# Performance work log

Hardware: AMD Instinct MI355X
Metric: run time of the kernel (lower is better)

## Reference

```python
import jax, jax.numpy as jnp
import numpy as np

L, B, H = 4096, 32, 512


def setup_inputs() -> dict:
    key = jax.random.key(0)
    k1, k2, k3, k4 = jax.random.split(key, 4)
    query = jax.random.normal(k1, (B, H), dtype=jnp.float32)
    key_val = jax.random.normal(k2, (L, B, H), dtype=jnp.float32)
    # torch Linear(2H, H, bias=False): weight is (H, 2H); we store transposed (2H, H)
    W = jax.random.normal(k3, (2 * H, H), dtype=jnp.float32) * (1.0 / np.sqrt(2 * H))
    v = jax.random.normal(k4, (H,), dtype=jnp.float32)
    return {"query": query, "key_val": key_val, "W": W, "v": v}


def reference(query, key_val, W, v):
    # concat([expand(query), key], -1) @ W == query @ W_q + key @ W_k
    Wq, Wk = W[:H], W[H:]                       # each (H, H)
    q_proj = query @ Wq                          # (B, H)
    k_proj = jnp.einsum('lbi,ih->lbh', key_val, Wk)  # (L, B, H)
    energy = jnp.tanh(q_proj[None, :, :] + k_proj)   # (L, B, H)
    scores = jnp.einsum('h,lbh->bl', v, energy)      # (B, L)
    return jax.nn.softmax(scores, axis=1)[:, None, :]  # (B, 1, L)
```

## Files before the change

kernel.cpp:

```cpp
#include <hip/hip_runtime.h>
#include <hip/hip_bf16.h>
#include <stdint.h>

#define L_DIM 4096
#define B_DIM 32
#define H_DIM 512
#define M_DIM (L_DIM * B_DIM)
#define K_DIM H_DIM

typedef _Float16 half8 __attribute__((ext_vector_type(8)));
typedef __fp16 fp16x2 __attribute__((ext_vector_type(2)));
typedef float floatx4 __attribute__((ext_vector_type(4)));

__device__ __forceinline__ float tanh_fast(float x) {
  float e = __builtin_amdgcn_exp2f(x * 2.88539008177793f);
  return 1.0f - 2.0f * __builtin_amdgcn_rcpf(e + 1.0f);
}

__device__ __forceinline__ uint2 pack4(const float4& f) {
  const fp16x2 p0 = __builtin_amdgcn_cvt_pkrtz(f.x, f.y);
  const fp16x2 p1 = __builtin_amdgcn_cvt_pkrtz(f.z, f.w);
  uint2 u;
  u.x = __builtin_bit_cast(unsigned, p0);
  u.y = __builtin_bit_cast(unsigned, p1);
  return u;
}

__global__ __launch_bounds__(128) void qproj_kernel(const float* __restrict__ query,
                                                    const float* __restrict__ W,
                                                    float* __restrict__ qp) {
  const int b = blockIdx.x;
  const int h = threadIdx.x * 4;
  const float* qrow = query + b * H_DIM;
  float4 acc = make_float4(0.f, 0.f, 0.f, 0.f);
#pragma unroll 8
  for (int i = 0; i < K_DIM; ++i) {
    const float qv = qrow[i];
    const float4 w4 = *(const float4*)(W + (size_t)i * H_DIM + h);
    acc.x += qv * w4.x; acc.y += qv * w4.y;
    acc.z += qv * w4.z; acc.w += qv * w4.w;
  }
  *(float4*)(qp + (size_t)b * H_DIM + h) = acc;
}

__global__ __launch_bounds__(256) void wconv_kernel(const float* __restrict__ W,
                                                    _Float16* __restrict__ W2) {
  const int t = blockIdx.x * 256 + threadIdx.x;
  const int l15 = t & 15;
  const int q = (t >> 4) & 3;
  const int nc = (t >> 6) & 31;
  const int kt = t >> 11;
  const int n = nc * 16 + l15;
  const int kbase = H_DIM + kt * 32 + q * 8;
  half8 h;
#pragma unroll
  for (int j = 0; j < 8; ++j)
    h[j] = (_Float16)W[(size_t)(kbase + j) * H_DIM + n];
  *(half8*)(W2 + (size_t)t * 8) = h;
}

__global__ __launch_bounds__(256, 2) void fused_gemm_kernel(
    const float* __restrict__ key, const _Float16* __restrict__ W2,
    const float* __restrict__ qp, const float* __restrict__ v,
    float* __restrict__ scores) {
  __shared__ __align__(16) _Float16 As[2][64 * 40];
  __shared__ float swave[256];

  const int tid = threadIdx.x;
  const int lane = tid & 63;
  const int w = tid >> 6;
  const int l15 = lane & 15;
  const int quad = lane >> 4;
  const int m0 = blockIdx.x * 64;

  const int ar = tid >> 3;
  const int aseg = tid & 7;
  const float* ag0 = key + (size_t)(m0 + ar) * K_DIM + aseg * 4;
  const float* ag1 = ag0 + (size_t)32 * K_DIM;
  const int adst0 = ar * 40 + aseg * 4;
  const int adst1 = (ar + 32) * 40 + aseg * 4;

  const half8* bptr = (const half8*)W2 + (size_t)(w * 8) * 64 + lane;

  int aoff[4];
#pragma unroll
  for (int fm = 0; fm < 4; ++fm) aoff[fm] = (fm * 16 + l15) * 40 + quad * 8;

  floatx4 acc[4][8];
#pragma unroll
  for (int fm = 0; fm < 4; ++fm)
#pragma unroll
    for (int fn = 0; fn < 8; ++fn) acc[fm][fn] = (floatx4)0.0f;

  float4 ra0 = *(const float4*)(ag0);
  float4 ra1 = *(const float4*)(ag1);
  half8 bn[8];
#pragma unroll
  for (int fn = 0; fn < 8; ++fn) bn[fn] = bptr[fn * 64];
  bptr += 32 * 64;
  *(uint2*)(As[0] + adst0) = pack4(ra0);
  *(uint2*)(As[0] + adst1) = pack4(ra1);
  ra0 = *(const float4*)(ag0 + 32);
  ra1 = *(const float4*)(ag1 + 32);
  __syncthreads();

  for (int kt = 0; kt < 16; ++kt) {
    half8 bc[8];
#pragma unroll
    for (int fn = 0; fn < 8; ++fn) bc[fn] = bn[fn];
    if (kt < 15) {
#pragma unroll
      for (int fn = 0; fn < 8; ++fn) bn[fn] = bptr[fn * 64];
      bptr += 32 * 64;
    }
    half8 av[4];
#pragma unroll
    for (int fm = 0; fm < 4; ++fm) av[fm] = *(const half8*)(As[kt & 1] + aoff[fm]);
    if (kt < 15) {
      _Float16* dst = As[(kt + 1) & 1];
      *(uint2*)(dst + adst0) = pack4(ra0);
      *(uint2*)(dst + adst1) = pack4(ra1);
      if (kt < 14) {
        ra0 = *(const float4*)(ag0 + (kt + 2) * 32);
        ra1 = *(const float4*)(ag1 + (kt + 2) * 32);
      }
    }
#pragma unroll
    for (int fm = 0; fm < 4; ++fm)
#pragma unroll
      for (int fn = 0; fn < 8; ++fn)
        acc[fm][fn] = __builtin_amdgcn_mfma_f32_16x16x32_f16(av[fm], bc[fn],
                                                             acc[fm][fn], 0, 0, 0);
    __syncthreads();
  }

  float vv[8];
#pragma unroll
  for (int fn = 0; fn < 8; ++fn) vv[fn] = v[w * 128 + fn * 16 + l15];

#pragma unroll
  for (int fm = 0; fm < 4; ++fm) {
#pragma unroll
    for (int r = 0; r < 4; ++r) {
      const int mrow = fm * 16 + quad * 4 + r;
      const float* qrow = qp + (size_t)(mrow & 31) * H_DIM;
      float rs = 0.f;
#pragma unroll
      for (int fn = 0; fn < 8; ++fn) {
        const int n = w * 128 + fn * 16 + l15;
        const float x = qrow[n] + acc[fm][fn][r];
        rs += vv[fn] * tanh_fast(x);
      }
      rs += __shfl_xor(rs, 1);
      rs += __shfl_xor(rs, 2);
      rs += __shfl_xor(rs, 4);
      rs += __shfl_xor(rs, 8);
      if (l15 == 0) swave[w * 64 + mrow] = rs;
    }
  }
  __syncthreads();
  if (tid < 64) {
    const float s = swave[tid] + swave[64 + tid] + swave[128 + tid] + swave[192 + tid];
    const int m = m0 + tid;
    scores[(size_t)(m & 31) * L_DIM + (m >> 5)] = s;
  }
}

__global__ __launch_bounds__(256) void softmax_kernel(const float* __restrict__ scores,
                                                      float* __restrict__ out) {
  const int b = blockIdx.x;
  const int t = threadIdx.x;
  __shared__ float red[256];
  const float* srow = scores + (size_t)b * L_DIM;
  float s[16];
#pragma unroll
  for (int i = 0; i < 16; ++i) s[i] = srow[t + i * 256];
  float mx = s[0];
#pragma unroll
  for (int i = 1; i < 16; ++i) mx = fmaxf(mx, s[i]);
  red[t] = mx;
  __syncthreads();
  for (int off = 128; off > 0; off >>= 1) {
    if (t < off) red[t] = fmaxf(red[t], red[t + off]);
    __syncthreads();
  }
  mx = red[0];
  __syncthreads();
  float sum = 0.f;
#pragma unroll
  for (int i = 0; i < 16; ++i) {
    s[i] = __builtin_amdgcn_exp2f((s[i] - mx) * 1.44269504f);
    sum += s[i];
  }
  red[t] = sum;
  __syncthreads();
  for (int off = 128; off > 0; off >>= 1) {
    if (t < off) red[t] += red[t + off];
    __syncthreads();
  }
  const float inv = 1.0f / red[0];
#pragma unroll
  for (int i = 0; i < 16; ++i) out[(size_t)b * L_DIM + t + i * 256] = s[i] * inv;
}

extern "C" void kernel_launch(void* const* d_in, const int* in_sizes, int n_in,
                              void* d_out, int out_size, void* d_ws, size_t ws_size,
                              hipStream_t stream) {
  const float* query = (const float*)d_in[0];
  const float* key   = (const float*)d_in[1];
  const float* W     = (const float*)d_in[2];
  const float* v     = (const float*)d_in[3];
  float* out = (float*)d_out;

  char* ws = (char*)d_ws;
  float* qp       = (float*)ws;
  float* scores   = (float*)(ws + 65536);
  _Float16* W2    = (_Float16*)(ws + 65536 + 524288);

  qproj_kernel<<<32, 128, 0, stream>>>(query, W, qp);
  wconv_kernel<<<128, 256, 0, stream>>>(W, W2);
  fused_gemm_kernel<<<M_DIM / 64, 256, 0, stream>>>(key, W2, qp, v, scores);
  softmax_kernel<<<B_DIM, 256, 0, stream>>>(scores, out);
}
```

Before: 446.7 us.

## Enlarge GEMM tile to 128 rows with 8 waves, merge prep kernels, shuffle softmax

The fused GEMM block grows from 64 to 128 rows and from 4 to 8 waves. Each wave now covers 64 output columns instead of 128, so the fp16 weight tile is loaded from L2 once per 128 rows rather than per 64. The query projection and weight conversion kernels are merged into one launch, and the softmax reductions switch from shared-memory trees to wavefront shuffles. In exchange, each block holds more LDS and more A-fragment registers, which may reduce occupancy.

```diff
diff --git a/kernel.cpp b/kernel.cpp
--- a/kernel.cpp
+++ b/kernel.cpp
@@ -26,77 +26,77 @@
   return u;
 }
 
-__global__ __launch_bounds__(128) void qproj_kernel(const float* __restrict__ query,
-                                                    const float* __restrict__ W,
-                                                    float* __restrict__ qp) {
-  const int b = blockIdx.x;
-  const int h = threadIdx.x * 4;
-  const float* qrow = query + b * H_DIM;
-  float4 acc = make_float4(0.f, 0.f, 0.f, 0.f);
+__global__ __launch_bounds__(256) void prep_kernel(const float* __restrict__ query,
+                                                   const float* __restrict__ W,
+                                                   float* __restrict__ qp,
+                                                   _Float16* __restrict__ W2) {
+  if (blockIdx.x < 128) {
+    const int t = blockIdx.x * 256 + threadIdx.x;
+    const int l15 = t & 15;
+    const int q = (t >> 4) & 3;
+    const int nc = (t >> 6) & 31;
+    const int kt = t >> 11;
+    const int n = nc * 16 + l15;
+    const int kbase = H_DIM + kt * 32 + q * 8;
+    half8 h;
+#pragma unroll
+    for (int j = 0; j < 8; ++j)
+      h[j] = (_Float16)W[(size_t)(kbase + j) * H_DIM + n];
+    *(half8*)(W2 + (size_t)t * 8) = h;
+  } else if (threadIdx.x < 128) {
+    const int b = blockIdx.x - 128;
+    const int h = threadIdx.x * 4;
+    const float* qrow = query + b * H_DIM;
+    float4 acc = make_float4(0.f, 0.f, 0.f, 0.f);
 #pragma unroll 8
-  for (int i = 0; i < K_DIM; ++i) {
-    const float qv = qrow[i];
-    const float4 w4 = *(const float4*)(W + (size_t)i * H_DIM + h);
-    acc.x += qv * w4.x; acc.y += qv * w4.y;
-    acc.z += qv * w4.z; acc.w += qv * w4.w;
-  }
-  *(float4*)(qp + (size_t)b * H_DIM + h) = acc;
-}
-
-__global__ __launch_bounds__(256) void wconv_kernel(const float* __restrict__ W,
-                                                    _Float16* __restrict__ W2) {
-  const int t = blockIdx.x * 256 + threadIdx.x;
-  const int l15 = t & 15;
-  const int q = (t >> 4) & 3;
-  const int nc = (t >> 6) & 31;
-  const int kt = t >> 11;
-  const int n = nc * 16 + l15;
-  const int kbase = H_DIM + kt * 32 + q * 8;
-  half8 h;
-#pragma unroll
-  for (int j = 0; j < 8; ++j)
-    h[j] = (_Float16)W[(size_t)(kbase + j) * H_DIM + n];
-  *(half8*)(W2 + (size_t)t * 8) = h;
-}
-
-__global__ __launch_bounds__(256, 2) void fused_gemm_kernel(
+    for (int i = 0; i < K_DIM; ++i) {
+      const float qv = qrow[i];
+      const float4 w4 = *(const float4*)(W + (size_t)i * H_DIM + h);
+      acc.x += qv * w4.x; acc.y += qv * w4.y;
+      acc.z += qv * w4.z; acc.w += qv * w4.w;
+    }
+    *(float4*)(qp + (size_t)b * H_DIM + h) = acc;
+  }
+}
+
+__global__ __launch_bounds__(512, 2) void fused_gemm_kernel(
     const float* __restrict__ key, const _Float16* __restrict__ W2,
     const float* __restrict__ qp, const float* __restrict__ v,
     float* __restrict__ scores) {
-  __shared__ __align__(16) _Float16 As[2][64 * 40];
-  __shared__ float swave[256];
+  __shared__ __align__(16) _Float16 As[2][128 * 40];
+  __shared__ float swave[8 * 128];
 
   const int tid = threadIdx.x;
   const int lane = tid & 63;
-  const int w = tid >> 6;
+  const int wn = tid >> 6;
   const int l15 = lane & 15;
   const int quad = lane >> 4;
-  const int m0 = blockIdx.x * 64;
+  const int m0 = blockIdx.x * 128;
 
   const int ar = tid >> 3;
   const int aseg = tid & 7;
   const float* ag0 = key + (size_t)(m0 + ar) * K_DIM + aseg * 4;
-  const float* ag1 = ag0 + (size_t)32 * K_DIM;
+  const float* ag1 = ag0 + (size_t)64 * K_DIM;
   const int adst0 = ar * 40 + aseg * 4;
-  const int adst1 = (ar + 32) * 40 + aseg * 4;
-
-  const half8* bptr = (const half8*)W2 + (size_t)(w * 8) * 64 + lane;
-
-  int aoff[4];
-#pragma unroll
-  for (int fm = 0; fm < 4; ++fm) aoff[fm] = (fm * 16 + l15) * 40 + quad * 8;
-
-  floatx4 acc[4][8];
-#pragma unroll
-  for (int fm = 0; fm < 4; ++fm)
-#pragma unroll
-    for (int fn = 0; fn < 8; ++fn) acc[fm][fn] = (floatx4)0.0f;
+  const int adst1 = (ar + 64) * 40 + aseg * 4;
+
+  const half8* bptr = (const half8*)W2 + (size_t)(wn * 4) * 64 + lane;
+
+  int aoff[8];
+#pragma unroll
+  for (int fm = 0; fm < 8; ++fm) aoff[fm] = (fm * 16 + l15) * 40 + quad * 8;
+
+  floatx4 acc[8][4];
+#pragma unroll
+  for (int fm = 0; fm < 8; ++fm)
+#pragma unroll
+    for (int fn = 0; fn < 4; ++fn) acc[fm][fn] = (floatx4)0.0f;
 
   float4 ra0 = *(const float4*)(ag0);
   float4 ra1 = *(const float4*)(ag1);
-  half8 bn[8];
-#pragma unroll
-  for (int fn = 0; fn < 8; ++fn) bn[fn] = bptr[fn * 64];
+  half8 bn[4];
+#pragma unroll
+  for (int fn = 0; fn < 4; ++fn) bn[fn] = bptr[fn * 64];
   bptr += 32 * 64;
   *(uint2*)(As[0] + adst0) = pack4(ra0);
   *(uint2*)(As[0] + adst1) = pack4(ra1);
@@ -105,17 +105,17 @@
   __syncthreads();
 
   for (int kt = 0; kt < 16; ++kt) {
-    half8 bc[8];
-#pragma unroll
-    for (int fn = 0; fn < 8; ++fn) bc[fn] = bn[fn];
+    half8 bc[4];
+#pragma unroll
+    for (int fn = 0; fn < 4; ++fn) bc[fn] = bn[fn];
     if (kt < 15) {
 #pragma unroll
-      for (int fn = 0; fn < 8; ++fn) bn[fn] = bptr[fn * 64];
+      for (int fn = 0; fn < 4; ++fn) bn[fn] = bptr[fn * 64];
       bptr += 32 * 64;
     }
-    half8 av[4];
-#pragma unroll
-    for (int fm = 0; fm < 4; ++fm) av[fm] = *(const half8*)(As[kt & 1] + aoff[fm]);
+    half8 av[8];
+#pragma unroll
+    for (int fm = 0; fm < 8; ++fm) av[fm] = *(const half8*)(As[kt & 1] + aoff[fm]);
     if (kt < 15) {
       _Float16* dst = As[(kt + 1) & 1];
       *(uint2*)(dst + adst0) = pack4(ra0);
@@ -126,28 +126,28 @@
       }
     }
 #pragma unroll
-    for (int fm = 0; fm < 4; ++fm)
-#pragma unroll
-      for (int fn = 0; fn < 8; ++fn)
+    for (int fm = 0; fm < 8; ++fm)
+#pragma unroll
+      for (int fn = 0; fn < 4; ++fn)
         acc[fm][fn] = __builtin_amdgcn_mfma_f32_16x16x32_f16(av[fm], bc[fn],
                                                              acc[fm][fn], 0, 0, 0);
     __syncthreads();
   }
 
-  float vv[8];
-#pragma unroll
-  for (int fn = 0; fn < 8; ++fn) vv[fn] = v[w * 128 + fn * 16 + l15];
-
-#pragma unroll
-  for (int fm = 0; fm < 4; ++fm) {
+  float vv[4];
+#pragma unroll
+  for (int fn = 0; fn < 4; ++fn) vv[fn] = v[wn * 64 + fn * 16 + l15];
+
+#pragma unroll
+  for (int fm = 0; fm < 8; ++fm) {
 #pragma unroll
     for (int r = 0; r < 4; ++r) {
       const int mrow = fm * 16 + quad * 4 + r;
       const float* qrow = qp + (size_t)(mrow & 31) * H_DIM;
       float rs = 0.f;
 #pragma unroll
-      for (int fn = 0; fn < 8; ++fn) {
-        const int n = w * 128 + fn * 16 + l15;
+      for (int fn = 0; fn < 4; ++fn) {
+        const int n = wn * 64 + fn * 16 + l15;
         const float x = qrow[n] + acc[fm][fn][r];
         rs += vv[fn] * tanh_fast(x);
       }
@@ -155,12 +155,14 @@
       rs += __shfl_xor(rs, 2);
       rs += __shfl_xor(rs, 4);
       rs += __shfl_xor(rs, 8);
-      if (l15 == 0) swave[w * 64 + mrow] = rs;
-    }
-  }
-  __syncthreads();
-  if (tid < 64) {
-    const float s = swave[tid] + swave[64 + tid] + swave[128 + tid] + swave[192 + tid];
+      if (l15 == 0) swave[wn * 128 + mrow] = rs;
+    }
+  }
+  __syncthreads();
+  if (tid < 128) {
+    float s = 0.f;
+#pragma unroll
+    for (int j = 0; j < 8; ++j) s += swave[j * 128 + tid];
     const int m = m0 + tid;
     scores[(size_t)(m & 31) * L_DIM + (m >> 5)] = s;
   }
@@ -170,7 +172,9 @@
                                                       float* __restrict__ out) {
   const int b = blockIdx.x;
   const int t = threadIdx.x;
-  __shared__ float red[256];
+  const int lane = t & 63;
+  const int w = t >> 6;
+  __shared__ float redm[4], reds[4];
   const float* srow = scores + (size_t)b * L_DIM;
   float s[16];
 #pragma unroll
@@ -178,27 +182,22 @@
   float mx = s[0];
 #pragma unroll
   for (int i = 1; i < 16; ++i) mx = fmaxf(mx, s[i]);
-  red[t] = mx;
-  __syncthreads();
-  for (int off = 128; off > 0; off >>= 1) {
-    if (t < off) red[t] = fmaxf(red[t], red[t + off]);
-    __syncthreads();
-  }
-  mx = red[0];
-  __syncthreads();
+#pragma unroll
+  for (int off = 1; off < 64; off <<= 1) mx = fmaxf(mx, __shfl_xor(mx, off));
+  if (lane == 0) redm[w] = mx;
+  __syncthreads();
+  mx = fmaxf(fmaxf(redm[0], redm[1]), fmaxf(redm[2], redm[3]));
   float sum = 0.f;
 #pragma unroll
   for (int i = 0; i < 16; ++i) {
     s[i] = __builtin_amdgcn_exp2f((s[i] - mx) * 1.44269504f);
     sum += s[i];
   }
-  red[t] = sum;
-  __syncthreads();
-  for (int off = 128; off > 0; off >>= 1) {
-    if (t < off) red[t] += red[t + off];
-    __syncthreads();
-  }
-  const float inv = 1.0f / red[0];
+#pragma unroll
+  for (int off = 1; off < 64; off <<= 1) sum += __shfl_xor(sum, off);
+  if (lane == 0) reds[w] = sum;
+  __syncthreads();
+  const float inv = 1.0f / (reds[0] + reds[1] + reds[2] + reds[3]);
 #pragma unroll
   for (int i = 0; i < 16; ++i) out[(size_t)b * L_DIM + t + i * 256] = s[i] * inv;
 }
@@ -217,8 +216,7 @@
   float* scores   = (float*)(ws + 65536);
   _Float16* W2    = (_Float16*)(ws + 65536 + 524288);
 
-  qproj_kernel<<<32, 128, 0, stream>>>(query, W, qp);
-  wconv_kernel<<<128, 256, 0, stream>>>(W, W2);
-  fused_gemm_kernel<<<M_DIM / 64, 256, 0, stream>>>(key, W2, qp, v, scores);
+  prep_kernel<<<160, 256, 0, stream>>>(query, W, qp, W2);
+  fused_gemm_kernel<<<M_DIM / 128, 512, 0, stream>>>(key, W2, qp, v, scores);
   softmax_kernel<<<B_DIM, 256, 0, stream>>>(scores, out);
 }
```

Result: no change. 449.0 us (+0.5%).
